# Optimization experiments

Hardware: AMD Instinct MI355X
Metric: run time of the kernel (lower is better)

The kernel has to match this reference:

```python
import jax, jax.numpy as jnp
import numpy as np

NUM_HEADS = 8


def setup_inputs() -> dict:
    key = jax.random.key(0)
    ks = jax.random.split(key, 7)
    b, t, prompt_dim, emb_dim = 2, 4096, 256, 512
    hidden = emb_dim  # head_dim=None -> hidden_dim = emb_dim
    def xavier(k, fan_in, fan_out):
        limit = np.sqrt(6.0 / (fan_in + fan_out)).astype(np.float32)
        return jax.random.uniform(k, (fan_in, fan_out), jnp.float32, -limit, limit)
    return {
        "prompt": jax.random.normal(ks[0], (b, t, prompt_dim), jnp.float32),
        "Wp": xavier(ks[1], prompt_dim, emb_dim),
        "bp": jnp.zeros((emb_dim,), jnp.float32),
        "Wqkv": xavier(ks[2], emb_dim, 3 * hidden),
        "bqkv": jnp.zeros((3 * hidden,), jnp.float32),
        "Wo": xavier(ks[3], hidden, prompt_dim),
        "bo": jnp.zeros((prompt_dim,), jnp.float32),
    }


def reference(prompt, Wp, bp, Wqkv, bqkv, Wo, bo):
    # prompt_proj
    x = prompt @ Wp + bp                      # [b, t, emb_dim]
    b, t, c = x.shape
    qkv = x @ Wqkv + bqkv                     # [b, t, 3*hidden]
    q, k, v = jnp.split(qkv, 3, axis=2)
    def to_heads(z):
        return z.reshape(b, t, NUM_HEADS, -1).transpose(0, 2, 1, 3)  # [b, h, t, d]
    q, k, v = to_heads(q), to_heads(k), to_heads(v)
    d = k.shape[-1]
    scores = jnp.einsum("bhid,bhjd->bhij", q, k) / jnp.sqrt(jnp.float32(d))
    attn = jax.nn.softmax(scores, axis=-1)    # dropout = identity (eval)
    out = jnp.einsum("bhij,bhjd->bhid", attn, v)
    out = out.transpose(0, 2, 1, 3).reshape(b, t, -1)  # [b, t, hidden]
    return out @ Wo + bo                      # [b, t, prompt_dim]
```

## Files before the change

### kernel.cpp

```cpp
#include <hip/hip_runtime.h>
#include <math.h>
#include <stdint.h>


typedef unsigned short u16;
typedef __attribute__((ext_vector_type(8))) __bf16 bf16x8;
typedef __attribute__((ext_vector_type(4))) __bf16 bf16x4;
typedef __attribute__((ext_vector_type(4))) float f32x4;

#define AS1 __attribute__((address_space(1)))
#define AS3 __attribute__((address_space(3)))

__device__ __forceinline__ void async16(const void* g, void* l) {
  __builtin_amdgcn_global_load_lds((const AS1 void*)g, (AS3 void*)l, 16, 0, 0);
}

__device__ __forceinline__ u16 f2bf(float f) {
  union { float f; unsigned u; } c; c.f = f;
  return (u16)((c.u + 0x7fffu + ((c.u >> 16) & 1u)) >> 16);
}

__global__ void prep_kernel(const float* __restrict__ prompt, u16* __restrict__ pbf,
                            const float* __restrict__ Wp, const float* __restrict__ Wqkv,
                            const float* __restrict__ Wo, u16* __restrict__ woT,
                            const float* __restrict__ bp, const float* __restrict__ bqkv,
                            float* __restrict__ bfused, u16* __restrict__ wfT) {
  __shared__ u16 Asf[64 * 40];
  __shared__ u16 Bsf[64 * 32];
  __shared__ float red[256];
  const int bid = blockIdx.x, tid = threadIdx.x;
  if (bid < 96) {
    const int k0 = (bid & 3) * 64, n0 = (bid >> 2) * 64;
    const int lane = tid & 63, w = tid >> 6;
    const int wr = w >> 1, wc = w & 1;
    const int lr = lane >> 4, lc = lane & 15;
    f32x4 acc[2][2];
#pragma unroll
    for (int a = 0; a < 2; a++)
#pragma unroll
      for (int b = 0; b < 2; b++) acc[a][b] = (f32x4){0.f, 0.f, 0.f, 0.f};
    for (int e0 = 0; e0 < 512; e0 += 32) {
      {
        const int er = tid >> 3, ng = (tid & 7) * 8;
        float4 v1 = *(const float4*)&Wqkv[(e0 + er) * 1536 + n0 + ng];
        float4 v2 = *(const float4*)&Wqkv[(e0 + er) * 1536 + n0 + ng + 4];
        Asf[(ng + 0) * 40 + er] = f2bf(v1.x); Asf[(ng + 1) * 40 + er] = f2bf(v1.y);
        Asf[(ng + 2) * 40 + er] = f2bf(v1.z); Asf[(ng + 3) * 40 + er] = f2bf(v1.w);
        Asf[(ng + 4) * 40 + er] = f2bf(v2.x); Asf[(ng + 5) * 40 + er] = f2bf(v2.y);
        Asf[(ng + 6) * 40 + er] = f2bf(v2.z); Asf[(ng + 7) * 40 + er] = f2bf(v2.w);
      }
      {
        const int kr = tid >> 2, ec = (tid & 3) * 8;
        float4 w1 = *(const float4*)&Wp[(k0 + kr) * 512 + e0 + ec];
        float4 w2 = *(const float4*)&Wp[(k0 + kr) * 512 + e0 + ec + 4];
        u16 tmp[8] = {f2bf(w1.x), f2bf(w1.y), f2bf(w1.z), f2bf(w1.w),
                      f2bf(w2.x), f2bf(w2.y), f2bf(w2.z), f2bf(w2.w)};
        *(uint4*)&Bsf[kr * 32 + ec] = *(const uint4*)&tmp[0];
      }
      __syncthreads();
      bf16x8 af[2], bf2[2];
#pragma unroll
      for (int mi = 0; mi < 2; mi++)
        af[mi] = *(const bf16x8*)&Asf[(wr * 32 + mi * 16 + lc) * 40 + lr * 8];
#pragma unroll
      for (int nj = 0; nj < 2; nj++)
        bf2[nj] = *(const bf16x8*)&Bsf[(wc * 32 + nj * 16 + lc) * 32 + lr * 8];
#pragma unroll
      for (int mi = 0; mi < 2; mi++)
#pragma unroll
        for (int nj = 0; nj < 2; nj++)
          acc[mi][nj] = __builtin_amdgcn_mfma_f32_16x16x32_bf16(af[mi], bf2[nj], acc[mi][nj], 0, 0, 0);
      __syncthreads();
    }
#pragma unroll
    for (int mi = 0; mi < 2; mi++)
#pragma unroll
      for (int nj = 0; nj < 2; nj++)
#pragma unroll
        for (int r = 0; r < 4; r++)
          wfT[(n0 + wr * 32 + mi * 16 + 4 * lr + r) * 256 + k0 + wc * 32 + nj * 16 + lc] =
              f2bf(acc[mi][nj][r]);
  } else if (bid < 120) {
    const int nloc = tid & 63, slice = tid >> 6;
    const int n = (bid - 96) * 64 + nloc;
    float s = 0.f;
#pragma unroll 8
    for (int e = slice * 128; e < slice * 128 + 128; e++) s += bp[e] * Wqkv[e * 1536 + n];
    red[tid] = s;
    __syncthreads();
    if (slice == 0)
      bfused[n] = red[nloc] + red[64 + nloc] + red[128 + nloc] + red[192 + nloc] + bqkv[n];
  } else if (bid < 632) {
    int j = (bid - 120) * 256 + tid;
    int n = j >> 9, k = j & 511;
    woT[j] = f2bf(Wo[k * 256 + n]);
  } else {
    int i = (bid - 632) * 256 + tid;
    float4 v = ((const float4*)prompt)[i];
    ushort4 o;
    o.x = f2bf(v.x); o.y = f2bf(v.y); o.z = f2bf(v.z); o.w = f2bf(v.w);
    ((ushort4*)pbf)[i] = o;
  }
}

__global__ __launch_bounds__(256) void gemm_qkv(
    const u16* __restrict__ A, const u16* __restrict__ Bt, const float* __restrict__ bias,
    u16* __restrict__ qO, u16* __restrict__ kO, u16* __restrict__ vO, int K) {
  constexpr int TM = 128, MI = 4, NJ = 4;
  __shared__ __align__(16) u16 As[2][TM * 32];
  __shared__ __align__(16) u16 Bs[2][TM * 32];
  const int tid = threadIdx.x;
  const int lane = tid & 63, w = tid >> 6;
  const int wr = w >> 1, wc = w & 1;
  const int lr = lane >> 4, lc = lane & 15;
  const long tileM = (long)blockIdx.y * 128;
  const long tileN = (long)blockIdx.x * 128;

  f32x4 acc[MI][NJ];
#pragma unroll
  for (int a = 0; a < MI; a++)
#pragma unroll
    for (int b = 0; b < NJ; b++) acc[a][b] = (f32x4){0.f, 0.f, 0.f, 0.f};

  const int r0 = lane >> 2;
  const int blk = lane & 3;

  auto stage = [&](int buf, int k0) {
#pragma unroll
    for (int i = 0; i < 2; i++) {
      int r = w * 32 + i * 16 + r0;
      int g = (blk ^ ((r >> 1) & 3)) << 3;
      async16(A + (tileM + r) * (long)K + k0 + g, (void*)&As[buf][(w * 32 + i * 16) * 32]);
      async16(Bt + (tileN + r) * (long)K + k0 + g, (void*)&Bs[buf][(w * 32 + i * 16) * 32]);
    }
  };

  stage(0, 0);
  for (int k0 = 0; k0 < K; k0 += 32) {
    const int cur = (k0 >> 5) & 1;
    stage(cur ^ 1, (k0 + 32 < K) ? k0 + 32 : 0);
    asm volatile("s_waitcnt vmcnt(4)" ::: "memory");
    asm volatile("s_barrier" ::: "memory");

    bf16x8 af[MI], bfv[NJ];
#pragma unroll
    for (int mi = 0; mi < MI; mi++) {
      int r = wr * 64 + mi * 16 + lc;
      af[mi] = *(const bf16x8*)&As[cur][r * 32 + ((lr ^ ((r >> 1) & 3)) << 3)];
    }
#pragma unroll
    for (int nj = 0; nj < NJ; nj++) {
      int r = wc * 64 + nj * 16 + lc;
      bfv[nj] = *(const bf16x8*)&Bs[cur][r * 32 + ((lr ^ ((r >> 1) & 3)) << 3)];
    }
#pragma unroll
    for (int mi = 0; mi < MI; mi++)
#pragma unroll
      for (int nj = 0; nj < NJ; nj++)
        acc[mi][nj] = __builtin_amdgcn_mfma_f32_16x16x32_bf16(af[mi], bfv[nj], acc[mi][nj], 0, 0, 0);
    asm volatile("s_barrier" ::: "memory");
  }

#pragma unroll
  for (int mi = 0; mi < MI; mi++)
#pragma unroll
    for (int nj = 0; nj < NJ; nj++) {
      long col = tileN + wc * 64 + nj * 16 + lc;
      float bcol = bias[col];
      long row0 = tileM + wr * 64 + mi * 16 + lr * 4;
      int sec = (int)(col >> 9);
      int c2 = (int)(col & 511);
      int h = c2 >> 6, d = c2 & 63;
      long pl = (row0 >> 12) * 8 + h;
      long t0 = row0 & 4095;
      if (sec == 2) {
        ushort4 pk;
        pk.x = f2bf(acc[mi][nj][0] + bcol);
        pk.y = f2bf(acc[mi][nj][1] + bcol);
        pk.z = f2bf(acc[mi][nj][2] + bcol);
        pk.w = f2bf(acc[mi][nj][3] + bcol);
        *(ushort4*)&vO[(pl * 64 + d) * 4096 + t0] = pk;
      } else {
        u16* dst = sec ? kO : qO;
        const float sc = sec ? 1.f : 0.18033688f;
#pragma unroll
        for (int r = 0; r < 4; r++)
          dst[((pl * 4096 + t0 + r) << 6) + d] = f2bf((acc[mi][nj][r] + bcol) * sc);
      }
    }
}

__global__ __launch_bounds__(256) void flash_attn(
    const u16* __restrict__ Q, const u16* __restrict__ Kg,
    const u16* __restrict__ VTg, u16* __restrict__ Og) {
  __shared__ __align__(16) u16 KV[3][8192];
  __shared__ __align__(16) u16 Ps[2][8192];

  const int tid = threadIdx.x, lane = tid & 63, w = tid >> 6;
  const int lr = lane >> 4, lc = lane & 15;
  const int plane = blockIdx.y;
  const long pbase = (long)plane << 18;
  const int qr0 = blockIdx.x * 128 + w * 32;

  bf16x8 bq[2][2];
#pragma unroll
  for (int qi = 0; qi < 2; qi++)
#pragma unroll
    for (int kk = 0; kk < 2; kk++)
      bq[qi][kk] = *(const bf16x8*)&Q[pbase + (long)(qr0 + qi * 16 + lc) * 64 + kk * 32 + lr * 8];

  bf16x8 ones;
#pragma unroll
  for (int u = 0; u < 8; u++) ones[u] = (__bf16)1.0f;

  f32x4 o[2][4], o1[2];
#pragma unroll
  for (int mi = 0; mi < 2; mi++) {
    o1[mi] = (f32x4){0.f, 0.f, 0.f, 0.f};
#pragma unroll
    for (int nj = 0; nj < 4; nj++) o[mi][nj] = (f32x4){0.f, 0.f, 0.f, 0.f};
  }

  const int krow = lane >> 3, kblk = lane & 7;

  auto stage = [&](int buf, int j) {
    const u16* kS = Kg + pbase + (long)j * 4096;
    const u16* vS = VTg + pbase + (long)j * 64;
#pragma unroll
    for (int i = 0; i < 2; i++) {
      int row = w * 16 + i * 8 + krow;
      async16(kS + (long)row * 64 + ((kblk ^ (row & 7)) << 3),
              (void*)&KV[buf][(w * 16 + i * 8) * 64]);
    }
#pragma unroll
    for (int i = 0; i < 2; i++) {
      int d = w * 16 + i * 8 + krow;
      async16(vS + (long)d * 4096 + ((kblk ^ (d & 7)) << 3),
              (void*)&KV[buf][4096 + (w * 16 + i * 8) * 64]);
    }
  };

  f32x4 s[4][2];

  auto compute_S = [&](int buf) {
#pragma unroll
    for (int ki = 0; ki < 4; ki++)
#pragma unroll
      for (int qi = 0; qi < 2; qi++) s[ki][qi] = (f32x4){0.f, 0.f, 0.f, 0.f};
    const u16* Ks = &KV[buf][0];
#pragma unroll
    for (int ki = 0; ki < 4; ki++) {
      const int row = ki * 16 + lc;
      bf16x8 ak[2];
#pragma unroll
      for (int kk = 0; kk < 2; kk++)
        ak[kk] = *(const bf16x8*)&Ks[row * 64 + (((kk * 4 + lr) ^ (row & 7)) << 3)];
#pragma unroll
      for (int qi = 0; qi < 2; qi++)
#pragma unroll
        for (int kk = 0; kk < 2; kk++)
          s[ki][qi] = __builtin_amdgcn_mfma_f32_16x16x32_bf16(ak[kk], bq[qi][kk], s[ki][qi], 0, 0, 0);
    }
  };

  auto pack_P = [&](int pbuf) {
#pragma unroll
    for (int qi = 0; qi < 2; qi++) {
      const int pb = w * 2048 + (qi * 16 + lc) * 64 + 4 * (lr & 1);
#pragma unroll
      for (int ki = 0; ki < 4; ki++) {
        bf16x4 pk;
        pk[0] = (__bf16)__builtin_amdgcn_exp2f(s[ki][qi][0]);
        pk[1] = (__bf16)__builtin_amdgcn_exp2f(s[ki][qi][1]);
        pk[2] = (__bf16)__builtin_amdgcn_exp2f(s[ki][qi][2]);
        pk[3] = (__bf16)__builtin_amdgcn_exp2f(s[ki][qi][3]);
        *(bf16x4*)&Ps[pbuf][pb + (((2 * ki + (lr >> 1)) ^ (lc & 7)) << 3)] = pk;
      }
    }
  };

  auto compute_PV = [&](int pbuf, int vbuf) {
    const u16* Vt = &KV[vbuf][4096];
#pragma unroll
    for (int kk = 0; kk < 2; kk++) {
      bf16x8 ap[2];
#pragma unroll
      for (int mi = 0; mi < 2; mi++)
        ap[mi] = *(const bf16x8*)&Ps[pbuf][w * 2048 + (mi * 16 + lc) * 64 + (((kk * 4 + lr) ^ (lc & 7)) << 3)];
#pragma unroll
      for (int nj = 0; nj < 4; nj++) {
        const int row = nj * 16 + lc;
        bf16x8 bv = *(const bf16x8*)&Vt[row * 64 + (((kk * 4 + lr) ^ (row & 7)) << 3)];
#pragma unroll
        for (int mi = 0; mi < 2; mi++)
          o[mi][nj] = __builtin_amdgcn_mfma_f32_16x16x32_bf16(ap[mi], bv, o[mi][nj], 0, 0, 0);
      }
#pragma unroll
      for (int mi = 0; mi < 2; mi++)
        o1[mi] = __builtin_amdgcn_mfma_f32_16x16x32_bf16(ap[mi], ones, o1[mi], 0, 0, 0);
    }
  };

  stage(0, 0);
  stage(1, 1);
  asm volatile("s_waitcnt vmcnt(4)" ::: "memory");
  asm volatile("s_barrier" ::: "memory");
  compute_S(0);
  pack_P(0);
  asm volatile("s_barrier" ::: "memory");

  for (int j = 1; j < 64; j++) {
    const int bj = j % 3;
    stage((j + 1) % 3, (j + 1 < 64) ? j + 1 : 0);
    asm volatile("s_waitcnt vmcnt(4)" ::: "memory");
    asm volatile("s_barrier" ::: "memory");
    compute_S(bj);
    compute_PV((j - 1) & 1, (j - 1) % 3);
    pack_P(j & 1);
    asm volatile("s_barrier" ::: "memory");
  }
  compute_PV(63 & 1, 63 % 3);

  const int bb = plane >> 3, h = plane & 7;
#pragma unroll
  for (int mi = 0; mi < 2; mi++)
#pragma unroll
    for (int r = 0; r < 4; r++) {
      float inv = 1.f / o1[mi][r];
      long t = qr0 + mi * 16 + 4 * lr + r;
#pragma unroll
      for (int nj = 0; nj < 4; nj++)
        Og[(((long)(bb * 4096 + t) * 8 + h) << 6) + nj * 16 + lc] = f2bf(o[mi][nj][r] * inv);
    }
}

__global__ __launch_bounds__(256) void gemm_out(
    const u16* __restrict__ A, const u16* __restrict__ Bt, const float* __restrict__ bias,
    float* __restrict__ outf) {
  constexpr int K = 512;
  __shared__ __align__(16) u16 As[2][64 * 32];
  __shared__ __align__(16) u16 Bs[2][64 * 32];
  const int tid = threadIdx.x;
  const int lane = tid & 63, w = tid >> 6;
  const int wr = w >> 1, wc = w & 1;
  const int lr = lane >> 4, lc = lane & 15;
  const long tileM = (long)blockIdx.y * 64;
  const long tileN = (long)blockIdx.x * 64;

  f32x4 acc[2][2];
#pragma unroll
  for (int a = 0; a < 2; a++)
#pragma unroll
    for (int b = 0; b < 2; b++) acc[a][b] = (f32x4){0.f, 0.f, 0.f, 0.f};

  const int r0 = lane >> 2;
  const int blk = lane & 3;

  auto stage = [&](int buf, int k0) {
    int r = w * 16 + r0;
    int g = (blk ^ ((r >> 1) & 3)) << 3;
    async16(A + (tileM + r) * (long)K + k0 + g, (void*)&As[buf][(w * 16) * 32]);
    async16(Bt + (tileN + r) * (long)K + k0 + g, (void*)&Bs[buf][(w * 16) * 32]);
  };

  stage(0, 0);
  for (int k0 = 0; k0 < K; k0 += 32) {
    const int cur = (k0 >> 5) & 1;
    stage(cur ^ 1, (k0 + 32 < K) ? k0 + 32 : 0);
    asm volatile("s_waitcnt vmcnt(2)" ::: "memory");
    asm volatile("s_barrier" ::: "memory");

    bf16x8 af[2], bfv[2];
#pragma unroll
    for (int mi = 0; mi < 2; mi++) {
      int r = wr * 32 + mi * 16 + lc;
      af[mi] = *(const bf16x8*)&As[cur][r * 32 + ((lr ^ ((r >> 1) & 3)) << 3)];
    }
#pragma unroll
    for (int nj = 0; nj < 2; nj++) {
      int r = wc * 32 + nj * 16 + lc;
      bfv[nj] = *(const bf16x8*)&Bs[cur][r * 32 + ((lr ^ ((r >> 1) & 3)) << 3)];
    }
#pragma unroll
    for (int mi = 0; mi < 2; mi++)
#pragma unroll
      for (int nj = 0; nj < 2; nj++)
        acc[mi][nj] = __builtin_amdgcn_mfma_f32_16x16x32_bf16(af[mi], bfv[nj], acc[mi][nj], 0, 0, 0);
    asm volatile("s_barrier" ::: "memory");
  }

#pragma unroll
  for (int mi = 0; mi < 2; mi++)
#pragma unroll
    for (int nj = 0; nj < 2; nj++) {
      long col = tileN + wc * 32 + nj * 16 + lc;
      float bcol = bias[col];
      long row0 = tileM + wr * 32 + mi * 16 + lr * 4;
#pragma unroll
      for (int r = 0; r < 4; r++)
        outf[(row0 + r) * 256 + col] = acc[mi][nj][r] + bcol;
    }
}

extern "C" void kernel_launch(void* const* d_in, const int* in_sizes, int n_in,
                              void* d_out, int out_size, void* d_ws, size_t ws_size,
                              hipStream_t stream) {
  const float* prompt = (const float*)d_in[0];
  const float* Wp = (const float*)d_in[1];
  const float* bp = (const float*)d_in[2];
  const float* Wqkv = (const float*)d_in[3];
  const float* bqkv = (const float*)d_in[4];
  const float* Wo = (const float*)d_in[5];
  const float* bo = (const float*)d_in[6];
  float* out = (float*)d_out;

  char* ws = (char*)d_ws;
  const size_t MiB = 1024 * 1024;
  u16* qb     = (u16*)(ws + 0);
  u16* kb     = (u16*)(ws + 8 * MiB);
  u16* vb     = (u16*)(ws + 16 * MiB);
  u16* pbf    = (u16*)(ws + 24 * MiB);
  u16* attnO  = (u16*)(ws + 28 * MiB);
  u16* woT    = (u16*)(ws + 36 * MiB);
  u16* wfT    = (u16*)(ws + 36 * MiB + 256 * 1024);
  float* bfused = (float*)(ws + 36 * MiB + 1024 * 1024);

  prep_kernel<<<dim3(2680), dim3(256), 0, stream>>>(
      prompt, pbf, Wp, Wqkv, Wo, woT, bp, bqkv, bfused, wfT);

  gemm_qkv<<<dim3(12, 64), dim3(256), 0, stream>>>(
      pbf, wfT, bfused, qb, kb, vb, 256);

  flash_attn<<<dim3(32, 16), dim3(256), 0, stream>>>(qb, kb, vb, attnO);

  gemm_out<<<dim3(4, 128), dim3(256), 0, stream>>>(attnO, woT, bo, out);
}
```

Before: 210.8 us.

## Split attention KV range across two blocks and merge partial sums

Flash attention now launches with a z-dimension of 2, each block covering half of the key range, so the grid grows from 512 to 1024 blocks to fill more CUs. Unnormalized partial outputs (bf16) and row sums are written to workspace, and a new reduce kernel adds the two halves and normalizes. The per-block pipeline is also reworked from a triple-buffered, software-pipelined S/PV schedule to a simpler double-buffered loop with a single P buffer. The split adds an extra kernel launch, extra global traffic, and an added bf16 rounding of partial outputs. It relies on there being no running max, since the scores are exponentiated directly.

```diff
diff --git a/kernel.cpp b/kernel.cpp
--- a/kernel.cpp
+++ b/kernel.cpp
@@ -18,6 +18,10 @@
 __device__ __forceinline__ u16 f2bf(float f) {
   union { float f; unsigned u; } c; c.f = f;
   return (u16)((c.u + 0x7fffu + ((c.u >> 16) & 1u)) >> 16);
+}
+
+__device__ __forceinline__ float bf2f(u16 u) {
+  union { unsigned x; float f; } z; z.x = (unsigned)u << 16; return z.f;
 }
 
 __global__ void prep_kernel(const float* __restrict__ prompt, u16* __restrict__ pbf,
@@ -192,15 +196,17 @@
 
 __global__ __launch_bounds__(256) void flash_attn(
     const u16* __restrict__ Q, const u16* __restrict__ Kg,
-    const u16* __restrict__ VTg, u16* __restrict__ Og) {
-  __shared__ __align__(16) u16 KV[3][8192];
-  __shared__ __align__(16) u16 Ps[2][8192];
+    const u16* __restrict__ VTg, u16* __restrict__ Op, float* __restrict__ lp) {
+  __shared__ __align__(16) u16 KV[2][8192];
+  __shared__ __align__(16) u16 Ps[4 * 2048];
 
   const int tid = threadIdx.x, lane = tid & 63, w = tid >> 6;
   const int lr = lane >> 4, lc = lane & 15;
   const int plane = blockIdx.y;
+  const int split = blockIdx.z;
   const long pbase = (long)plane << 18;
   const int qr0 = blockIdx.x * 128 + w * 32;
+  const int tj0 = split * 32;
 
   bf16x8 bq[2][2];
 #pragma unroll
@@ -223,9 +229,9 @@
 
   const int krow = lane >> 3, kblk = lane & 7;
 
-  auto stage = [&](int buf, int j) {
-    const u16* kS = Kg + pbase + (long)j * 4096;
-    const u16* vS = VTg + pbase + (long)j * 64;
+  auto stage = [&](int buf, int tj) {
+    const u16* kS = Kg + pbase + (long)tj * 4096;
+    const u16* vS = VTg + pbase + (long)tj * 64;
 #pragma unroll
     for (int i = 0; i < 2; i++) {
       int row = w * 16 + i * 8 + krow;
@@ -240,14 +246,21 @@
     }
   };
 
-  f32x4 s[4][2];
-
-  auto compute_S = [&](int buf) {
+  stage(0, tj0);
+  for (int j = 0; j < 32; j++) {
+    const int cur = j & 1;
+    stage(cur ^ 1, (j + 1 < 32) ? tj0 + j + 1 : tj0);
+    asm volatile("s_waitcnt vmcnt(4)" ::: "memory");
+    asm volatile("s_barrier" ::: "memory");
+
+    const u16* Ks = &KV[cur][0];
+    const u16* Vt = &KV[cur][4096];
+
+    f32x4 s[4][2];
 #pragma unroll
     for (int ki = 0; ki < 4; ki++)
 #pragma unroll
       for (int qi = 0; qi < 2; qi++) s[ki][qi] = (f32x4){0.f, 0.f, 0.f, 0.f};
-    const u16* Ks = &KV[buf][0];
 #pragma unroll
     for (int ki = 0; ki < 4; ki++) {
       const int row = ki * 16 + lc;
@@ -261,9 +274,7 @@
         for (int kk = 0; kk < 2; kk++)
           s[ki][qi] = __builtin_amdgcn_mfma_f32_16x16x32_bf16(ak[kk], bq[qi][kk], s[ki][qi], 0, 0, 0);
     }
-  };
-
-  auto pack_P = [&](int pbuf) {
+
 #pragma unroll
     for (int qi = 0; qi < 2; qi++) {
       const int pb = w * 2048 + (qi * 16 + lc) * 64 + 4 * (lr & 1);
@@ -274,19 +285,16 @@
         pk[1] = (__bf16)__builtin_amdgcn_exp2f(s[ki][qi][1]);
         pk[2] = (__bf16)__builtin_amdgcn_exp2f(s[ki][qi][2]);
         pk[3] = (__bf16)__builtin_amdgcn_exp2f(s[ki][qi][3]);
-        *(bf16x4*)&Ps[pbuf][pb + (((2 * ki + (lr >> 1)) ^ (lc & 7)) << 3)] = pk;
+        *(bf16x4*)&Ps[pb + (((2 * ki + (lr >> 1)) ^ (lc & 7)) << 3)] = pk;
       }
     }
-  };
-
-  auto compute_PV = [&](int pbuf, int vbuf) {
-    const u16* Vt = &KV[vbuf][4096];
+
 #pragma unroll
     for (int kk = 0; kk < 2; kk++) {
       bf16x8 ap[2];
 #pragma unroll
       for (int mi = 0; mi < 2; mi++)
-        ap[mi] = *(const bf16x8*)&Ps[pbuf][w * 2048 + (mi * 16 + lc) * 64 + (((kk * 4 + lr) ^ (lc & 7)) << 3)];
+        ap[mi] = *(const bf16x8*)&Ps[w * 2048 + (mi * 16 + lc) * 64 + (((kk * 4 + lr) ^ (lc & 7)) << 3)];
 #pragma unroll
       for (int nj = 0; nj < 4; nj++) {
         const int row = nj * 16 + lc;
@@ -299,39 +307,40 @@
       for (int mi = 0; mi < 2; mi++)
         o1[mi] = __builtin_amdgcn_mfma_f32_16x16x32_bf16(ap[mi], ones, o1[mi], 0, 0, 0);
     }
-  };
-
-  stage(0, 0);
-  stage(1, 1);
-  asm volatile("s_waitcnt vmcnt(4)" ::: "memory");
-  asm volatile("s_barrier" ::: "memory");
-  compute_S(0);
-  pack_P(0);
-  asm volatile("s_barrier" ::: "memory");
-
-  for (int j = 1; j < 64; j++) {
-    const int bj = j % 3;
-    stage((j + 1) % 3, (j + 1 < 64) ? j + 1 : 0);
-    asm volatile("s_waitcnt vmcnt(4)" ::: "memory");
-    asm volatile("s_barrier" ::: "memory");
-    compute_S(bj);
-    compute_PV((j - 1) & 1, (j - 1) % 3);
-    pack_P(j & 1);
     asm volatile("s_barrier" ::: "memory");
   }
-  compute_PV(63 & 1, 63 % 3);
 
   const int bb = plane >> 3, h = plane & 7;
+  u16* Ob = Op + (long)split * 4194304;
 #pragma unroll
   for (int mi = 0; mi < 2; mi++)
 #pragma unroll
     for (int r = 0; r < 4; r++) {
-      float inv = 1.f / o1[mi][r];
       long t = qr0 + mi * 16 + 4 * lr + r;
 #pragma unroll
       for (int nj = 0; nj < 4; nj++)
-        Og[(((long)(bb * 4096 + t) * 8 + h) << 6) + nj * 16 + lc] = f2bf(o[mi][nj][r] * inv);
-    }
+        Ob[(((long)(bb * 4096 + t) * 8 + h) << 6) + nj * 16 + lc] = f2bf(o[mi][nj][r]);
+      if (lc == 0) lp[((split * 16 + plane) << 12) + t] = o1[mi][r];
+    }
+}
+
+__global__ void reduce_kernel(u16* __restrict__ Op, const float* __restrict__ lp) {
+  int i = blockIdx.x * 256 + threadIdx.x;
+  int row = i >> 7;
+  int c4 = (i & 127) << 2;
+  int h = c4 >> 6;
+  int b = row >> 12, t = row & 4095;
+  float l = lp[((b * 8 + h) << 12) + t] + lp[65536 + ((b * 8 + h) << 12) + t];
+  float inv = 1.f / l;
+  long idx = (long)row * 512 + c4;
+  ushort4 a = *(const ushort4*)&Op[idx];
+  ushort4 c = *(const ushort4*)&Op[4194304 + idx];
+  ushort4 o;
+  o.x = f2bf((bf2f(a.x) + bf2f(c.x)) * inv);
+  o.y = f2bf((bf2f(a.y) + bf2f(c.y)) * inv);
+  o.z = f2bf((bf2f(a.z) + bf2f(c.z)) * inv);
+  o.w = f2bf((bf2f(a.w) + bf2f(c.w)) * inv);
+  *(ushort4*)&Op[idx] = o;
 }
 
 __global__ __launch_bounds__(256) void gemm_out(
@@ -420,10 +429,11 @@
   u16* kb     = (u16*)(ws + 8 * MiB);
   u16* vb     = (u16*)(ws + 16 * MiB);
   u16* pbf    = (u16*)(ws + 24 * MiB);
-  u16* attnO  = (u16*)(ws + 28 * MiB);
-  u16* woT    = (u16*)(ws + 36 * MiB);
-  u16* wfT    = (u16*)(ws + 36 * MiB + 256 * 1024);
-  float* bfused = (float*)(ws + 36 * MiB + 1024 * 1024);
+  float* lpp  = (float*)(ws + 24 * MiB);
+  u16* Op     = (u16*)(ws + 28 * MiB);
+  u16* woT    = (u16*)(ws + 44 * MiB);
+  u16* wfT    = (u16*)(ws + 44 * MiB + 256 * 1024);
+  float* bfused = (float*)(ws + 45 * MiB);
 
   prep_kernel<<<dim3(2680), dim3(256), 0, stream>>>(
       prompt, pbf, Wp, Wqkv, Wo, woT, bp, bqkv, bfused, wfT);
@@ -431,7 +441,9 @@
   gemm_qkv<<<dim3(12, 64), dim3(256), 0, stream>>>(
       pbf, wfT, bfused, qb, kb, vb, 256);
 
-  flash_attn<<<dim3(32, 16), dim3(256), 0, stream>>>(qb, kb, vb, attnO);
-
-  gemm_out<<<dim3(4, 128), dim3(256), 0, stream>>>(attnO, woT, bo, out);
-}
+  flash_attn<<<dim3(32, 16, 2), dim3(256), 0, stream>>>(qb, kb, vb, Op, lpp);
+
+  reduce_kernel<<<dim3(4096), dim3(256), 0, stream>>>(Op, lpp);
+
+  gemm_out<<<dim3(4, 128), dim3(256), 0, stream>>>(Op, woT, bo, out);
+}
```

After: 207.5 us. About the same (-1.6%).
